# Kernel optimization log

Hardware: AMD Instinct MI355X
Metric: run time of the kernel (lower is better)

## Reference

```python
import jax, jax.numpy as jnp
import numpy as np

IN_FEATURES_LS = (64, 128, 256, 512)
OUT_FEATURES = 1024
MAX_FEAT = max(IN_FEATURES_LS)
N_TOKENS = 65536


def setup_inputs() -> dict:
    key = jax.random.key(0)
    kx, kg, kw, kb = jax.random.split(key, 4)
    x = jax.random.normal(kx, (N_TOKENS, MAX_FEAT), dtype=jnp.float32)
    gidx = jax.random.randint(kg, (N_TOKENS,), 0, len(IN_FEATURES_LS))
    # per-sample declared input size; values are exactly entries of IN_FEATURES_LS
    in_feat_size = jnp.asarray(IN_FEATURES_LS, dtype=jnp.int64 if jax.config.jax_enable_x64 else jnp.int32)[gidx]
    weight = jax.random.normal(kw, (len(IN_FEATURES_LS), OUT_FEATURES, MAX_FEAT), dtype=jnp.float32) * 0.02
    bias = jax.random.normal(kb, (len(IN_FEATURES_LS), OUT_FEATURES), dtype=jnp.float32) * 0.02
    return {"x": x, "in_feat_size": in_feat_size, "weight": weight, "bias": bias}


def reference(x, in_feat_size, weight, bias):
    # mask[g, i] = i < in_features_ls[g]; zero out padded weight columns
    sizes = jnp.asarray(IN_FEATURES_LS, dtype=jnp.int32)
    feat_mask = (jnp.arange(MAX_FEAT)[None, :] < sizes[:, None]).astype(x.dtype)  # [G, max_feat]
    out = jnp.zeros(x.shape[:-1] + (OUT_FEATURES,), dtype=x.dtype)
    for idx, feat_size in enumerate(IN_FEATURES_LS):
        w = weight[idx] * feat_mask[idx][None, :]          # [out, max_feat]
        y = jnp.einsum('oi,ni->no', w, x) + bias[idx]       # [N, out]
        sel = (in_feat_size == feat_size).astype(x.dtype)[..., None]
        out = out + sel * y
    return out
```

## Files before the change

### kernel.cpp

```cpp
#include <hip/hip_runtime.h>
#include <hip/hip_bf16.h>

#define N_TOKENS 65536
#define MAXF 512
#define OUTF 1024
#define NGROUP 4

typedef __attribute__((ext_vector_type(8))) short short8;
typedef __attribute__((ext_vector_type(4))) float floatx4;
typedef unsigned short ushort_t;
typedef unsigned int uint_t;

__device__ __forceinline__ uint_t f2bf(float f) {
    uint_t u = __float_as_uint(f);
    u += 0x7fffu + ((u >> 16) & 1u);
    return u >> 16;
}

#define OFF_CNT    0
#define OFF_LISTS  16384
#define OFF_XB     (2u<<20)
#define OFF_WB     ((2u<<20) + ((size_t)N_TOKENS*MAXF*2))
#define WS_FULL    (OFF_WB + (size_t)NGROUP*OUTF*MAXF*2)
#define WS_MIN     (OFF_LISTS + (size_t)NGROUP*N_TOKENS*4)

__global__ void prep_kernel(const int* __restrict__ sizes, int* __restrict__ cnt,
                            int* __restrict__ lists) {
    __shared__ int wcnt[4][NGROUP];
    __shared__ int gbase[NGROUP];
    int t = threadIdx.x, wave = t >> 6, lane = t & 63;
    int tok = blockIdx.x * 256 + t;
    int g = __ffs(sizes[tok]) - 7;
    int pos = 0;
    #pragma unroll
    for (int gg = 0; gg < NGROUP; ++gg) {
        unsigned long long m = __ballot(g == gg);
        if (g == gg) pos = __popcll(m & ((1ull << lane) - 1ull));
        if (lane == 0) wcnt[wave][gg] = __popcll(m);
    }
    __syncthreads();
    if (t < NGROUP) {
        int tot = wcnt[0][t] + wcnt[1][t] + wcnt[2][t] + wcnt[3][t];
        gbase[t] = atomicAdd(&cnt[t], tot);
    }
    __syncthreads();
    int off = gbase[g];
    for (int w = 0; w < wave; ++w) off += wcnt[w][g];
    lists[(g << 16) + off + pos] = tok;
}

__global__ void conv_kernel(const float* __restrict__ x, const float* __restrict__ weight,
                            const int* __restrict__ cnt, const int* __restrict__ lists,
                            ushort_t* __restrict__ xb, ushort_t* __restrict__ wb) {
    int c0 = cnt[0], c1 = cnt[1], c2 = cnt[2], c3 = cnt[3];
    int p1 = c0 << 3;
    int p2 = p1 + (c1 << 4);
    int p3 = p2 + (c2 << 5);
    int xT = p3 + (c3 << 6);
    int T = 122880 + xT;
    int xs1 = c0 << 6;
    int xs2 = xs1 + (c1 << 7);
    int xs3 = xs2 + (c2 << 8);
    int stride = gridDim.x * blockDim.x;
    for (int id = blockIdx.x * blockDim.x + threadIdx.x; id < T; id += stride) {
        const floatx4* src;
        ushort_t* dst;
        if (id < 122880) {
            int g, local, wsb;
            if (id < 8192)       { g = 0; local = id;         wsb = 0;      }
            else if (id < 24576) { g = 1; local = id - 8192;  wsb = 65536;  }
            else if (id < 57344) { g = 2; local = id - 24576; wsb = 196608; }
            else                 { g = 3; local = id - 57344; wsb = 458752; }
            int shift = 3 + g;
            int row = local >> shift;
            int k = (local - (row << shift)) << 3;
            src = (const floatx4*)(weight + (size_t)g * OUTF * MAXF + (size_t)row * MAXF + k);
            dst = wb + wsb + ((size_t)row << (6 + g)) + k;
        } else {
            int xid = id - 122880;
            int g, local, xs;
            if (xid < p1)      { g = 0; local = xid;      xs = 0;   }
            else if (xid < p2) { g = 1; local = xid - p1; xs = xs1; }
            else if (xid < p3) { g = 2; local = xid - p2; xs = xs2; }
            else               { g = 3; local = xid - p3; xs = xs3; }
            int shift = 3 + g;
            int sl = local >> shift;
            int k = (local - (sl << shift)) << 3;
            int tok = lists[(g << 16) + sl];
            src = (const floatx4*)(x + (size_t)tok * MAXF + k);
            dst = xb + (size_t)xs + ((size_t)sl << (6 + g)) + k;
        }
        floatx4 a = src[0], b = src[1];
        short8 v;
        v[0] = (short)f2bf(a[0]); v[1] = (short)f2bf(a[1]);
        v[2] = (short)f2bf(a[2]); v[3] = (short)f2bf(a[3]);
        v[4] = (short)f2bf(b[0]); v[5] = (short)f2bf(b[1]);
        v[6] = (short)f2bf(b[2]); v[7] = (short)f2bf(b[3]);
        *(short8*)dst = v;
    }
}

#define GLOAD_LDS16(gptr, lptr)                                                \
    __builtin_amdgcn_global_load_lds(                                          \
        (const __attribute__((address_space(1))) uint_t*)(gptr),               \
        (__attribute__((address_space(3))) uint_t*)(lptr), 16, 0, 0)

__global__ __launch_bounds__(512, 1) void gemm_bf16_kernel(
    const ushort_t* __restrict__ xb, const ushort_t* __restrict__ wb,
    const float* __restrict__ bias, const int* __restrict__ cnt,
    const int* __restrict__ lists, float* __restrict__ out) {

    extern __shared__ char sh[];

    const int c0 = cnt[0], c1 = cnt[1], c2 = cnt[2], c3 = cnt[3];
    const int T3 = ((c3 + 255) >> 8) << 2;
    const int T2 = ((c2 + 255) >> 8) << 2;
    const int T1 = ((c1 + 255) >> 8) << 2;
    const int T0 = ((c0 + 255) >> 8) << 2;
    const int tcount = T3 + T2 + T1 + T0;
    const int xs1 = c0 << 6;
    const int xs2 = xs1 + (c1 << 7);
    const int xs3 = xs2 + (c2 << 8);

    int id = blockIdx.x;
    if (id >= tcount) return;

    {
        int q = tcount >> 3, r = tcount & 7;
        int xcd = id & 7, idx = id >> 3;
        id = ((xcd < r) ? xcd * (q + 1) : r * (q + 1) + (xcd - r) * q) + idx;
    }

    int g, local, count, xs, wsb;
    if (id < T3)                { g = 3; local = id;                count = c3; xs = xs3; wsb = 458752; }
    else if (id < T3 + T2)      { g = 2; local = id - T3;           count = c2; xs = xs2; wsb = 196608; }
    else if (id < T3 + T2 + T1) { g = 1; local = id - T3 - T2;      count = c1; xs = xs1; wsb = 65536;  }
    else                        { g = 0; local = id - T3 - T2 - T1; count = c0; xs = 0;   wsb = 0;      }

    const int mt = local >> 2, nt = local & 3;
    const int m_base = mt << 8;
    const int n_base = nt << 8;
    const int K_log = 6 + g;
    const int nsteps = 1 << (g + 1);
    const int rows = min(256, count - m_base);

    const int t = threadIdx.x;
    const int wave = t >> 6, lane = t & 63;
    const int wm = wave >> 2, wn = wave & 3;
    const int quad = lane >> 4, l16 = lane & 15;
    const int rsub = lane >> 2;
    const int kq = (((lane & 3) ^ ((lane >> 3) & 3)) << 3);
    const int rp = (l16 >> 1) & 3;

    int* oidx = (int*)(sh + 98304);

    if (t < 256) {
        int m = m_base + t;
        oidx[t] = (m < count) ? lists[(g << 16) + m] : 0;
    }
    float bvreg[4];
    #pragma unroll
    for (int ni = 0; ni < 4; ++ni)
        bvreg[ni] = bias[g * OUTF + n_base + wn * 64 + ni * 16 + l16];

    const ushort_t* aptr[2];
    const ushort_t* bptr[2];
    #pragma unroll
    for (int j = 0; j < 2; ++j) {
        int br = wave * 32 + j * 16;
        int ar = min(m_base + br + rsub, count - 1);
        aptr[j] = xb + (size_t)xs + ((size_t)ar << K_log) + kq;
        bptr[j] = wb + (size_t)wsb + ((size_t)(n_base + br + rsub) << K_log) + kq;
    }

    floatx4 acc[8][4];
    #pragma unroll
    for (int i = 0; i < 8; ++i)
        #pragma unroll
        for (int j = 0; j < 4; ++j) acc[i][j] = (floatx4)(0.0f);

    asm volatile("s_waitcnt vmcnt(0)" ::: "memory");

    #pragma unroll
    for (int j = 0; j < 2; ++j) {
        int br = wave * 32 + j * 16;
        GLOAD_LDS16(aptr[j], sh + br * 64);
        GLOAD_LDS16(bptr[j], sh + 16384 + br * 64);
    }
    #pragma unroll
    for (int j = 0; j < 2; ++j) {
        int br = wave * 32 + j * 16;
        GLOAD_LDS16(aptr[j] + 32, sh + 32768 + br * 64);
        GLOAD_LDS16(bptr[j] + 32, sh + 32768 + 16384 + br * 64);
    }

    int buf = 0;
    for (int s = 0; s < nsteps; ++s) {
        if (s + 1 < nsteps)
            asm volatile("s_waitcnt vmcnt(4) lgkmcnt(0)" ::: "memory");
        else
            asm volatile("s_waitcnt vmcnt(0) lgkmcnt(0)" ::: "memory");
        __builtin_amdgcn_s_barrier();
        asm volatile("" ::: "memory");

        const ushort_t* Ab = (const ushort_t*)(sh + buf * 32768);
        const ushort_t* Bb = (const ushort_t*)(sh + buf * 32768 + 16384);
        short8 af[8], bfr[4];
        #pragma unroll
        for (int mi = 0; mi < 8; ++mi)
            af[mi] = *(const short8*)&Ab[(wm * 128 + mi * 16 + l16) * 32 + ((quad ^ rp) << 3)];
        #pragma unroll
        for (int ni = 0; ni < 4; ++ni)
            bfr[ni] = *(const short8*)&Bb[(wn * 64 + ni * 16 + l16) * 32 + ((quad ^ rp) << 3)];

        #pragma unroll
        for (int mi = 0; mi < 8; ++mi)
            #pragma unroll
            for (int ni = 0; ni < 4; ++ni)
                acc[mi][ni] = __builtin_amdgcn_mfma_f32_16x16x32_bf16(
                    af[mi], bfr[ni], acc[mi][ni], 0, 0, 0);

        if (s + 2 < nsteps) {
            int k0 = (s + 2) << 5;
            int bn = buf + 2; if (bn >= 3) bn -= 3;
            char* dstA = sh + bn * 32768;
            #pragma unroll
            for (int j = 0; j < 2; ++j) {
                int br = wave * 32 + j * 16;
                GLOAD_LDS16(aptr[j] + k0, dstA + br * 64);
                GLOAD_LDS16(bptr[j] + k0, dstA + 16384 + br * 64);
            }
        }
        buf = (buf == 2) ? 0 : buf + 1;
    }

    __syncthreads();

    float* shf = (float*)sh;
    #pragma unroll
    for (int c = 0; c < 4; ++c) {
        if (wm == (c >> 1)) {
            int mi0 = (c & 1) * 4;
            #pragma unroll
            for (int mm = 0; mm < 4; ++mm) {
                #pragma unroll
                for (int ni = 0; ni < 4; ++ni) {
                    int col = wn * 64 + ni * 16 + l16;
                    #pragma unroll
                    for (int r = 0; r < 4; ++r) {
                        int lrow = mm * 16 + quad * 4 + r;
                        shf[lrow * 260 + col] = acc[mi0 + mm][ni][r] + bvreg[ni];
                    }
                }
            }
        }
        __syncthreads();
        #pragma unroll
        for (int k = 0; k < 8; ++k) {
            int idx = t + k * 512;
            int row = idx >> 6;
            int f4  = idx & 63;
            int m = c * 64 + row;
            if (m < rows) {
                floatx4 v = *(const floatx4*)&shf[row * 260 + f4 * 4];
                __builtin_nontemporal_store(
                    v, (floatx4*)&out[(size_t)oidx[m] * OUTF + n_base + f4 * 4]);
            }
        }
        __syncthreads();
    }
}

__global__ __launch_bounds__(256) void gemm_fp32_kernel(
    const float* __restrict__ x, const float* __restrict__ weight,
    const float* __restrict__ bias, const int* __restrict__ cnt,
    const int* __restrict__ lists, float* __restrict__ out) {

    const int g = blockIdx.z;
    const int count = cnt[g];
    const int m_base = blockIdx.y * 128;
    if (m_base >= count) return;
    const int n_base = blockIdx.x * 128;
    const int K = 64 << g;
    const int rows = min(128, count - m_base);

    __shared__ ushort_t As[128][40];
    __shared__ ushort_t Bs[128][40];
    __shared__ int idxs[128];

    const int t = threadIdx.x;
    if (t < 128) idxs[t] = (t < rows) ? lists[(g << 16) + m_base + t]
                                      : lists[(g << 16) + m_base];
    __syncthreads();

    const int wave = t >> 6, lane = t & 63;
    const int wm = wave >> 1, wn = wave & 1;
    const int quad = lane >> 4, l16 = lane & 15;

    floatx4 acc[4][4];
    #pragma unroll
    for (int i = 0; i < 4; ++i)
        #pragma unroll
        for (int j = 0; j < 4; ++j) acc[i][j] = (floatx4)(0.0f);

    const float* wg = weight + (size_t)g * OUTF * MAXF;

    for (int k0 = 0; k0 < K; k0 += 32) {
        #pragma unroll
        for (int rep = 0; rep < 4; ++rep) {
            int id = t + rep * 256;
            int row = id >> 3;
            int kqq = id & 7;
            floatx4 av = *(const floatx4*)(x + (size_t)idxs[row] * MAXF + k0 + kqq * 4);
            unsigned long long pa = (unsigned long long)f2bf(av[0]) |
                ((unsigned long long)f2bf(av[1]) << 16) |
                ((unsigned long long)f2bf(av[2]) << 32) |
                ((unsigned long long)f2bf(av[3]) << 48);
            *(unsigned long long*)&As[row][kqq * 4] = pa;
            floatx4 bvv = *(const floatx4*)(wg + (size_t)(n_base + row) * MAXF + k0 + kqq * 4);
            unsigned long long pb = (unsigned long long)f2bf(bvv[0]) |
                ((unsigned long long)f2bf(bvv[1]) << 16) |
                ((unsigned long long)f2bf(bvv[2]) << 32) |
                ((unsigned long long)f2bf(bvv[3]) << 48);
            *(unsigned long long*)&Bs[row][kqq * 4] = pb;
        }
        __syncthreads();

        short8 af[4], bfr[4];
        #pragma unroll
        for (int mi = 0; mi < 4; ++mi)
            af[mi] = *(const short8*)&As[wm * 64 + mi * 16 + l16][quad * 8];
        #pragma unroll
        for (int ni = 0; ni < 4; ++ni)
            bfr[ni] = *(const short8*)&Bs[wn * 64 + ni * 16 + l16][quad * 8];
        #pragma unroll
        for (int mi = 0; mi < 4; ++mi)
            #pragma unroll
            for (int ni = 0; ni < 4; ++ni)
                acc[mi][ni] = __builtin_amdgcn_mfma_f32_16x16x32_bf16(
                    af[mi], bfr[ni], acc[mi][ni], 0, 0, 0);
        __syncthreads();
    }

    #pragma unroll
    for (int ni = 0; ni < 4; ++ni) {
        int col = n_base + wn * 64 + ni * 16 + l16;
        float bv = bias[g * OUTF + col];
        #pragma unroll
        for (int mi = 0; mi < 4; ++mi) {
            int mloc = wm * 64 + mi * 16 + quad * 4;
            #pragma unroll
            for (int r = 0; r < 4; ++r) {
                int m = mloc + r;
                if (m < rows)
                    out[(size_t)idxs[m] * OUTF + col] = acc[mi][ni][r] + bv;
            }
        }
    }
}

extern "C" void kernel_launch(void* const* d_in, const int* in_sizes, int n_in,
                              void* d_out, int out_size, void* d_ws, size_t ws_size,
                              hipStream_t stream) {
    const float* x      = (const float*)d_in[0];
    const int*   sizes  = (const int*)d_in[1];
    const float* weight = (const float*)d_in[2];
    const float* bias   = (const float*)d_in[3];
    float* out = (float*)d_out;

    char* ws = (char*)d_ws;
    int* cnt   = (int*)(ws + OFF_CNT);
    int* lists = (int*)(ws + OFF_LISTS);
    ushort_t* xb = (ushort_t*)(ws + OFF_XB);
    ushort_t* wb = (ushort_t*)(ws + OFF_WB);

    hipMemsetAsync(ws + OFF_CNT, 0, NGROUP * sizeof(int), stream);
    prep_kernel<<<N_TOKENS / 256, 256, 0, stream>>>(sizes, cnt, lists);

    if (ws_size >= WS_FULL) {
        static int attr_done = 0;
        if (!attr_done) {
            hipFuncSetAttribute((const void*)gemm_bf16_kernel,
                                hipFuncAttributeMaxDynamicSharedMemorySize, 99328);
            attr_done = 1;
        }
        conv_kernel<<<2048, 256, 0, stream>>>(x, weight, cnt, lists, xb, wb);
        gemm_bf16_kernel<<<1036, 512, 99328, stream>>>(xb, wb, bias, cnt, lists, out);
    } else {
        dim3 grid(OUTF / 128, N_TOKENS / 128, NGROUP);
        gemm_fp32_kernel<<<grid, 256, 0, stream>>>(x, weight, bias, cnt, lists, out);
    }
}
```

Measured before the change: 415.1 us.

## Halve GEMM N-tile to 128 and use static LDS for higher occupancy

```diff
diff --git a/kernel.cpp b/kernel.cpp
--- a/kernel.cpp
+++ b/kernel.cpp
@@ -105,18 +105,18 @@
         (const __attribute__((address_space(1))) uint_t*)(gptr),               \
         (__attribute__((address_space(3))) uint_t*)(lptr), 16, 0, 0)
 
-__global__ __launch_bounds__(512, 1) void gemm_bf16_kernel(
+__global__ __launch_bounds__(512, 4) void gemm_bf16_kernel(
     const ushort_t* __restrict__ xb, const ushort_t* __restrict__ wb,
     const float* __restrict__ bias, const int* __restrict__ cnt,
     const int* __restrict__ lists, float* __restrict__ out) {
 
-    extern __shared__ char sh[];
+    __shared__ __align__(16) char sh[50176];
 
     const int c0 = cnt[0], c1 = cnt[1], c2 = cnt[2], c3 = cnt[3];
-    const int T3 = ((c3 + 255) >> 8) << 2;
-    const int T2 = ((c2 + 255) >> 8) << 2;
-    const int T1 = ((c1 + 255) >> 8) << 2;
-    const int T0 = ((c0 + 255) >> 8) << 2;
+    const int T3 = ((c3 + 255) >> 8) << 3;
+    const int T2 = ((c2 + 255) >> 8) << 3;
+    const int T1 = ((c1 + 255) >> 8) << 3;
+    const int T0 = ((c0 + 255) >> 8) << 3;
     const int tcount = T3 + T2 + T1 + T0;
     const int xs1 = c0 << 6;
     const int xs2 = xs1 + (c1 << 7);
@@ -137,22 +137,21 @@
     else if (id < T3 + T2 + T1) { g = 1; local = id - T3 - T2;      count = c1; xs = xs1; wsb = 65536;  }
     else                        { g = 0; local = id - T3 - T2 - T1; count = c0; xs = 0;   wsb = 0;      }
 
-    const int mt = local >> 2, nt = local & 3;
+    const int mt = local >> 3, nt = local & 7;
     const int m_base = mt << 8;
-    const int n_base = nt << 8;
+    const int n_base = nt << 7;
     const int K_log = 6 + g;
     const int nsteps = 1 << (g + 1);
     const int rows = min(256, count - m_base);
 
     const int t = threadIdx.x;
     const int wave = t >> 6, lane = t & 63;
-    const int wm = wave >> 2, wn = wave & 3;
+    const int wm = wave >> 1, wn = wave & 1;
     const int quad = lane >> 4, l16 = lane & 15;
     const int rsub = lane >> 2;
-    const int kq = (((lane & 3) ^ ((lane >> 3) & 3)) << 3);
-    const int rp = (l16 >> 1) & 3;
-
-    int* oidx = (int*)(sh + 98304);
+    const int kq = (lane & 3) * 8;
+
+    int* oidx = (int*)(sh + 49152);
 
     if (t < 256) {
         int m = m_base + t;
@@ -163,106 +162,86 @@
     for (int ni = 0; ni < 4; ++ni)
         bvreg[ni] = bias[g * OUTF + n_base + wn * 64 + ni * 16 + l16];
 
-    const ushort_t* aptr[2];
-    const ushort_t* bptr[2];
-    #pragma unroll
-    for (int j = 0; j < 2; ++j) {
-        int br = wave * 32 + j * 16;
-        int ar = min(m_base + br + rsub, count - 1);
-        aptr[j] = xb + (size_t)xs + ((size_t)ar << K_log) + kq;
-        bptr[j] = wb + (size_t)wsb + ((size_t)(n_base + br + rsub) << K_log) + kq;
-    }
-
-    floatx4 acc[8][4];
-    #pragma unroll
-    for (int i = 0; i < 8; ++i)
+    const ushort_t* a0;
+    const ushort_t* a1;
+    const ushort_t* b0;
+    {
+        int r0 = min(m_base + wave * 32 + rsub, count - 1);
+        int r1 = min(m_base + wave * 32 + 16 + rsub, count - 1);
+        a0 = xb + (size_t)xs + ((size_t)r0 << K_log) + kq;
+        a1 = xb + (size_t)xs + ((size_t)r1 << K_log) + kq;
+        int br = n_base + wave * 16 + rsub;
+        b0 = wb + (size_t)wsb + ((size_t)br << K_log) + kq;
+    }
+
+    floatx4 acc[4][4];
+    #pragma unroll
+    for (int i = 0; i < 4; ++i)
         #pragma unroll
         for (int j = 0; j < 4; ++j) acc[i][j] = (floatx4)(0.0f);
 
-    asm volatile("s_waitcnt vmcnt(0)" ::: "memory");
-
-    #pragma unroll
-    for (int j = 0; j < 2; ++j) {
-        int br = wave * 32 + j * 16;
-        GLOAD_LDS16(aptr[j], sh + br * 64);
-        GLOAD_LDS16(bptr[j], sh + 16384 + br * 64);
-    }
-    #pragma unroll
-    for (int j = 0; j < 2; ++j) {
-        int br = wave * 32 + j * 16;
-        GLOAD_LDS16(aptr[j] + 32, sh + 32768 + br * 64);
-        GLOAD_LDS16(bptr[j] + 32, sh + 32768 + 16384 + br * 64);
-    }
+    GLOAD_LDS16(a0, sh + (wave * 32) * 64);
+    GLOAD_LDS16(a1, sh + (wave * 32 + 16) * 64);
+    GLOAD_LDS16(b0, sh + 16384 + wave * 16 * 64);
+    __syncthreads();
 
     int buf = 0;
     for (int s = 0; s < nsteps; ++s) {
-        if (s + 1 < nsteps)
-            asm volatile("s_waitcnt vmcnt(4) lgkmcnt(0)" ::: "memory");
-        else
-            asm volatile("s_waitcnt vmcnt(0) lgkmcnt(0)" ::: "memory");
-        __builtin_amdgcn_s_barrier();
-        asm volatile("" ::: "memory");
-
-        const ushort_t* Ab = (const ushort_t*)(sh + buf * 32768);
-        const ushort_t* Bb = (const ushort_t*)(sh + buf * 32768 + 16384);
-        short8 af[8], bfr[4];
-        #pragma unroll
-        for (int mi = 0; mi < 8; ++mi)
-            af[mi] = *(const short8*)&Ab[(wm * 128 + mi * 16 + l16) * 32 + ((quad ^ rp) << 3)];
+        if (s + 1 < nsteps) {
+            int k0 = (s + 1) << 5;
+            char* d = sh + (buf ^ 1) * 24576;
+            GLOAD_LDS16(a0 + k0, d + (wave * 32) * 64);
+            GLOAD_LDS16(a1 + k0, d + (wave * 32 + 16) * 64);
+            GLOAD_LDS16(b0 + k0, d + 16384 + wave * 16 * 64);
+        }
+
+        const ushort_t* Ab = (const ushort_t*)(sh + buf * 24576);
+        const ushort_t* Bb = (const ushort_t*)(sh + buf * 24576 + 16384);
+        short8 af[4], bfr[4];
+        #pragma unroll
+        for (int mi = 0; mi < 4; ++mi)
+            af[mi] = *(const short8*)&Ab[(wm * 64 + mi * 16 + l16) * 32 + quad * 8];
         #pragma unroll
         for (int ni = 0; ni < 4; ++ni)
-            bfr[ni] = *(const short8*)&Bb[(wn * 64 + ni * 16 + l16) * 32 + ((quad ^ rp) << 3)];
-
-        #pragma unroll
-        for (int mi = 0; mi < 8; ++mi)
+            bfr[ni] = *(const short8*)&Bb[(wn * 64 + ni * 16 + l16) * 32 + quad * 8];
+
+        #pragma unroll
+        for (int mi = 0; mi < 4; ++mi)
             #pragma unroll
             for (int ni = 0; ni < 4; ++ni)
                 acc[mi][ni] = __builtin_amdgcn_mfma_f32_16x16x32_bf16(
                     af[mi], bfr[ni], acc[mi][ni], 0, 0, 0);
 
-        if (s + 2 < nsteps) {
-            int k0 = (s + 2) << 5;
-            int bn = buf + 2; if (bn >= 3) bn -= 3;
-            char* dstA = sh + bn * 32768;
+        __syncthreads();
+        buf ^= 1;
+    }
+
+    float* shf = (float*)sh;
+    #pragma unroll
+    for (int c = 0; c < 4; ++c) {
+        if (wm == c) {
             #pragma unroll
-            for (int j = 0; j < 2; ++j) {
-                int br = wave * 32 + j * 16;
-                GLOAD_LDS16(aptr[j] + k0, dstA + br * 64);
-                GLOAD_LDS16(bptr[j] + k0, dstA + 16384 + br * 64);
-            }
-        }
-        buf = (buf == 2) ? 0 : buf + 1;
-    }
-
-    __syncthreads();
-
-    float* shf = (float*)sh;
-    #pragma unroll
-    for (int c = 0; c < 4; ++c) {
-        if (wm == (c >> 1)) {
-            int mi0 = (c & 1) * 4;
-            #pragma unroll
-            for (int mm = 0; mm < 4; ++mm) {
+            for (int mi = 0; mi < 4; ++mi) {
                 #pragma unroll
                 for (int ni = 0; ni < 4; ++ni) {
                     int col = wn * 64 + ni * 16 + l16;
                     #pragma unroll
                     for (int r = 0; r < 4; ++r) {
-                        int lrow = mm * 16 + quad * 4 + r;
-                        shf[lrow * 260 + col] = acc[mi0 + mm][ni][r] + bvreg[ni];
+                        int lrow = mi * 16 + quad * 4 + r;
+                        shf[lrow * 132 + col] = acc[mi][ni][r] + bvreg[ni];
                     }
                 }
             }
         }
         __syncthreads();
         #pragma unroll
-        for (int k = 0; k < 8; ++k) {
+        for (int k = 0; k < 4; ++k) {
             int idx = t + k * 512;
-            int row = idx >> 6;
-            int f4  = idx & 63;
+            int row = idx >> 5;
+            int f4  = idx & 31;
             int m = c * 64 + row;
             if (m < rows) {
-                floatx4 v = *(const floatx4*)&shf[row * 260 + f4 * 4];
+                floatx4 v = *(const floatx4*)&shf[row * 132 + f4 * 4];
                 __builtin_nontemporal_store(
                     v, (floatx4*)&out[(size_t)oidx[m] * OUTF + n_base + f4 * 4]);
             }
@@ -378,14 +357,8 @@
     prep_kernel<<<N_TOKENS / 256, 256, 0, stream>>>(sizes, cnt, lists);
 
     if (ws_size >= WS_FULL) {
-        static int attr_done = 0;
-        if (!attr_done) {
-            hipFuncSetAttribute((const void*)gemm_bf16_kernel,
-                                hipFuncAttributeMaxDynamicSharedMemorySize, 99328);
-            attr_done = 1;
-        }
         conv_kernel<<<2048, 256, 0, stream>>>(x, weight, cnt, lists, xb, wb);
-        gemm_bf16_kernel<<<1036, 512, 99328, stream>>>(xb, wb, bias, cnt, lists, out);
+        gemm_bf16_kernel<<<2080, 512, 0, stream>>>(xb, wb, bias, cnt, lists, out);
     } else {
         dim3 grid(OUTF / 128, N_TOKENS / 128, NGROUP);
         gemm_fp32_kernel<<<grid, 256, 0, stream>>>(x, weight, bias, cnt, lists, out);
```

Measured after the change: 408.7 us. Within noise of the previous version (-1.5%).
